# Optimization experiments

Measured on AMD Instinct MI355X. Metric: run time of the kernel, lower is better.

Reference implementation:

```python
import jax, jax.numpy as jnp
import numpy as np

EPS = 1e-8
WINDOW = 3      # config.router_window_size
TEMP = 1.0      # config.router_temp (> 0, so sqrt(D) fallback unused)
TOP_K = 2       # config.moe_top_k


def _routing_weights(x, prototypes):
    # L2-normalize router input per token (normalize_router_input=True)
    x = x / jnp.clip(jnp.linalg.norm(x, axis=-1, keepdims=True), EPS)
    # 'window' mode: causal moving average of size WINDOW along seq, with the
    # first token replicated WINDOW-1 times on the left (matches F.conv1d with
    # left pad of flat_input[:, :, [0]] and an averaging kernel).
    w = WINDOW
    padded = jnp.concatenate([jnp.repeat(x[:, :1], w - 1, axis=1), x], axis=1)  # [B, S+w-1, D]
    cs = jnp.concatenate(
        [jnp.zeros_like(padded[:, :1]), jnp.cumsum(padded, axis=1)], axis=1
    )  # [B, S+w, D]
    router_input = (cs[:, w:] - cs[:, :-w]) / w  # [B, S, D] moving mean
    # F.linear(router_input, prototypes): logits over experts
    logits = jnp.einsum('bsd,ed->bse', router_input, prototypes)  # [B, S, E]
    # softmax in float32 (F.softmax(..., dtype=torch.float))
    return jax.nn.softmax((logits / TEMP).astype(jnp.float32), axis=-1)


def setup_inputs() -> dict:
    key = jax.random.key(0)
    k1, k2 = jax.random.split(key)
    bs, sq, D, E = 8, 2048, 1024, 64
    x = jax.random.normal(k1, (bs, sq, D), dtype=jnp.float32)
    prototypes = jax.random.normal(k2, (E, D), dtype=jnp.float32) * 0.02
    attn_mask = jnp.ones((bs, sq), dtype=jnp.int32)
    return {"x": x, "prototypes": prototypes, "attn_mask": attn_mask}


def reference(x, prototypes, attn_mask):
    # attn_mask is all ones here; in 'window' mode it only feeds logging stats.
    routing_weights = _routing_weights(x, prototypes)          # [B, S, E]
    weights, modules = jax.lax.top_k(routing_weights, TOP_K)   # [B, S, K]
    weights = weights / weights.sum(axis=-1, keepdims=True)    # renormalize top-k
    return modules, weights
```

## Files before the change

kernel.cpp:

```cpp
#include <hip/hip_runtime.h>
#include <math.h>


#define BB 8
#define SS 2048
#define DD 1024
#define EE 64
#define EPSV 1e-8f

#define FMA4(A, s, P) \
  A.x += (s) * (P).x; A.y += (s) * (P).y; A.z += (s) * (P).z; A.w += (s) * (P).w;

__global__ __launch_bounds__(256) void repack_proto(
    const float* __restrict__ proto, float* __restrict__ ptt) {
  const int gid = blockIdx.x * 256 + threadIdx.x;
  const int d = gid >> 6;
  const int e = gid & 63;
  ptt[gid] = proto[(size_t)e * DD + d];
}

__global__ __launch_bounds__(256, 2) void router_dots(
    const float* __restrict__ x, const float* __restrict__ ptt,
    float* __restrict__ dots) {
  __shared__ float xt[4][16][36];
  __shared__ float B0[32][68];
  __shared__ float B1[32][68];
  __shared__ float nq[4][32];

  const int lane = threadIdx.x & 63;
  const int w    = __builtin_amdgcn_readfirstlane(threadIdx.x >> 6);
  const int b    = blockIdx.x >> 6;
  const int s0   = (blockIdx.x & 63) * 32;

  const int toks = lane & 31;
  const int kh   = lane >> 5;
  const int eg   = lane & 7;
  const int tg   = lane >> 3;

  const float* xb = x + ((size_t)b * SS + s0) * DD;
  const int kbase = w * 256;

  float4 acc0[4], acc1[4];
#pragma unroll
  for (int i = 0; i < 4; ++i) {
    acc0[i] = make_float4(0.f, 0.f, 0.f, 0.f);
    acc1[i] = make_float4(0.f, 0.f, 0.f, 0.f);
  }
  float q = 0.0f;

  for (int c = 0; c < 16; ++c) {
    const int dof = kbase + c * 16;
    const float* xs = xb + (size_t)toks * DD + dof + kh * 8;
    const float4 v0 = *(const float4*)(xs);
    const float4 v1 = *(const float4*)(xs + 4);
    q += v0.x * v0.x + v0.y * v0.y + v0.z * v0.z + v0.w * v0.w +
         v1.x * v1.x + v1.y * v1.y + v1.z * v1.z + v1.w * v1.w;
    xt[w][kh * 8 + 0][toks] = v0.x;
    xt[w][kh * 8 + 1][toks] = v0.y;
    xt[w][kh * 8 + 2][toks] = v0.z;
    xt[w][kh * 8 + 3][toks] = v0.w;
    xt[w][kh * 8 + 4][toks] = v1.x;
    xt[w][kh * 8 + 5][toks] = v1.y;
    xt[w][kh * 8 + 6][toks] = v1.z;
    xt[w][kh * 8 + 7][toks] = v1.w;
#pragma unroll
    for (int kk = 0; kk < 16; ++kk) {
      const float4 xf = *(const float4*)(&xt[w][kk][tg * 4]);
      const float* pr = ptt + (size_t)(dof + kk) * EE + eg * 8;
      const float4 p0 = *(const float4*)(pr);
      const float4 p1 = *(const float4*)(pr + 4);
      FMA4(acc0[0], xf.x, p0) FMA4(acc1[0], xf.x, p1)
      FMA4(acc0[1], xf.y, p0) FMA4(acc1[1], xf.y, p1)
      FMA4(acc0[2], xf.z, p0) FMA4(acc1[2], xf.z, p1)
      FMA4(acc0[3], xf.w, p0) FMA4(acc1[3], xf.w, p1)
    }
  }

  q += __shfl_xor(q, 32);
  if (kh == 0) nq[w][toks] = q;

#define WRB(B)                                                  \
  { _Pragma("unroll") for (int i = 0; i < 4; ++i) {             \
      *(float4*)(&(B)[tg * 4 + i][eg * 8])     = acc0[i];       \
      *(float4*)(&(B)[tg * 4 + i][eg * 8 + 4]) = acc1[i]; } }
#define ADDB(B)                                                 \
  { _Pragma("unroll") for (int i = 0; i < 4; ++i) {             \
      const float4 t0 = *(const float4*)(&(B)[tg * 4 + i][eg * 8]);     \
      const float4 t1 = *(const float4*)(&(B)[tg * 4 + i][eg * 8 + 4]); \
      acc0[i].x += t0.x; acc0[i].y += t0.y;                     \
      acc0[i].z += t0.z; acc0[i].w += t0.w;                     \
      acc1[i].x += t1.x; acc1[i].y += t1.y;                     \
      acc1[i].z += t1.z; acc1[i].w += t1.w; } }

  __syncthreads();
  if (w == 1) WRB(B0)
  if (w == 3) WRB(B1)
  __syncthreads();
  if (w == 0) ADDB(B0)
  if (w == 2) ADDB(B1)
  __syncthreads();
  if (w == 2) WRB(B0)
  __syncthreads();
  if (w == 0) {
    ADDB(B0)
#pragma unroll
    for (int i = 0; i < 4; ++i) {
      const int row = tg * 4 + i;
      const float qs = nq[0][row] + nq[1][row] + nq[2][row] + nq[3][row];
      const float inv = 1.0f / fmaxf(sqrtf(qs), EPSV);
      float4 o0, o1;
      o0.x = acc0[i].x * inv; o0.y = acc0[i].y * inv;
      o0.z = acc0[i].z * inv; o0.w = acc0[i].w * inv;
      o1.x = acc1[i].x * inv; o1.y = acc1[i].y * inv;
      o1.z = acc1[i].z * inv; o1.w = acc1[i].w * inv;
      float* dp = dots + ((size_t)b * SS + s0 + row) * EE + eg * 8;
      *(float4*)(dp)     = o0;
      *(float4*)(dp + 4) = o1;
    }
  }
}

#define T2UP(s, ei)                                            \
  if ((s) > v1) { v2 = v1; i2 = i1; v1 = (s); i1 = (ei); }     \
  else if ((s) > v2) { v2 = (s); i2 = (ei); }

__global__ __launch_bounds__(256) void router_top2(
    const float* __restrict__ dots, float* __restrict__ out) {
  const int gtid = blockIdx.x * 256 + threadIdx.x;
  const int tok  = gtid >> 1;
  const int h    = gtid & 1;
  const int b    = tok >> 11;
  const int sl   = tok & (SS - 1);
  const int r0   = (sl >= 2) ? sl - 2 : 0;
  const int r1   = (sl >= 1) ? sl - 1 : 0;

  const float* d0 = dots + ((size_t)b * SS + r0) * EE + h * 32;
  const float* d1 = dots + ((size_t)b * SS + r1) * EE + h * 32;
  const float* d2 = dots + ((size_t)b * SS + sl) * EE + h * 32;

  float v1 = -INFINITY, v2 = -INFINITY;
  int i1 = 0, i2 = 0;
#pragma unroll
  for (int qd = 0; qd < 8; ++qd) {
    const float4 a = *(const float4*)(d0 + qd * 4);
    const float4 c = *(const float4*)(d1 + qd * 4);
    const float4 e = *(const float4*)(d2 + qd * 4);
    const int e0 = h * 32 + qd * 4;
    float s;
    s = a.x + c.x + e.x; T2UP(s, e0 + 0)
    s = a.y + c.y + e.y; T2UP(s, e0 + 1)
    s = a.z + c.z + e.z; T2UP(s, e0 + 2)
    s = a.w + c.w + e.w; T2UP(s, e0 + 3)
  }

  {
    const float ov1 = __shfl_xor(v1, 1);
    const int   oi1 = __shfl_xor(i1, 1);
    const float ov2 = __shfl_xor(v2, 1);
    const int   oi2 = __shfl_xor(i2, 1);
    const bool o_beats = (ov1 > v1) || (ov1 == v1 && oi1 < i1);
    if (o_beats) {
      const bool v1_beats_o2 = (v1 > ov2) || (v1 == ov2 && i1 < oi2);
      v2 = v1_beats_o2 ? v1 : ov2;
      i2 = v1_beats_o2 ? i1 : oi2;
      v1 = ov1;
      i1 = oi1;
    } else {
      const bool o1_beats_v2 = (ov1 > v2) || (ov1 == v2 && oi1 < i2);
      if (o1_beats_v2) { v2 = ov1; i2 = oi1; }
    }
  }

  if (h == 0) {
    const float ex = expf((v2 - v1) * (1.0f / 3.0f));
    const float w1 = 1.0f / (1.0f + ex);
    const size_t o = (size_t)tok * 2;
    *(float2*)(out + o) = make_float2((float)i1, (float)i2);
    *(float2*)(out + (size_t)BB * SS * 2 + o) = make_float2(w1, ex * w1);
  }
}

extern "C" void kernel_launch(void* const* d_in, const int* in_sizes, int n_in,
                              void* d_out, int out_size, void* d_ws, size_t ws_size,
                              hipStream_t stream) {
  const float* x     = (const float*)d_in[0];
  const float* proto = (const float*)d_in[1];
  float* out  = (float*)d_out;
  float* ptt  = (float*)d_ws;
  float* dots = (float*)((char*)d_ws + (512 << 10));

  repack_proto<<<dim3(256), dim3(256), 0, stream>>>(proto, ptt);
  router_dots<<<dim3(512), dim3(256), 0, stream>>>(x, ptt, dots);
  router_top2<<<dim3(128), dim3(256), 0, stream>>>(dots, out);
}
```

Before: 136.1 us.

## Split K across 8 waves with double-buffered x tiles and prototype prefetch

The dot kernel now runs 512 threads per block, splitting the 1024-wide reduction over 8 waves of 128 columns each instead of 4 waves of 256. Each wave double-buffers its transposed x tile in shared memory, loading the next chunk while computing the current one. It also keeps a 4-deep register ring of prototype rows prefetched ahead of use. The goal is to hide global load latency and raise the number of waves in flight, at the cost of a deeper cross-wave reduction tree with more barriers and more register and LDS pressure.

```diff
diff --git a/kernel.cpp b/kernel.cpp
--- a/kernel.cpp
+++ b/kernel.cpp
@@ -8,8 +8,14 @@
 #define EE 64
 #define EPSV 1e-8f
 
+#define NW 8
+#define KSL 128
+#define NCHK 8
+
 #define FMA4(A, s, P) \
   A.x += (s) * (P).x; A.y += (s) * (P).y; A.z += (s) * (P).z; A.w += (s) * (P).w;
+
+#define SUMSQ4(v) ((v).x * (v).x + (v).y * (v).y + (v).z * (v).z + (v).w * (v).w)
 
 __global__ __launch_bounds__(256) void repack_proto(
     const float* __restrict__ proto, float* __restrict__ ptt) {
@@ -19,13 +25,12 @@
   ptt[gid] = proto[(size_t)e * DD + d];
 }
 
-__global__ __launch_bounds__(256, 2) void router_dots(
+__global__ __launch_bounds__(512, 4) void router_dots(
     const float* __restrict__ x, const float* __restrict__ ptt,
     float* __restrict__ dots) {
-  __shared__ float xt[4][16][36];
-  __shared__ float B0[32][68];
-  __shared__ float B1[32][68];
-  __shared__ float nq[4][32];
+  __shared__ float xt[NW][2][16][36];
+  __shared__ float B[4][32][68];
+  __shared__ float nq[NW][32];
 
   const int lane = threadIdx.x & 63;
   const int w    = __builtin_amdgcn_readfirstlane(threadIdx.x >> 6);
@@ -38,7 +43,7 @@
   const int tg   = lane >> 3;
 
   const float* xb = x + ((size_t)b * SS + s0) * DD;
-  const int kbase = w * 256;
+  const int kbase = w * KSL;
 
   float4 acc0[4], acc1[4];
 #pragma unroll
@@ -48,65 +53,105 @@
   }
   float q = 0.0f;
 
-  for (int c = 0; c < 16; ++c) {
-    const int dof = kbase + c * 16;
-    const float* xs = xb + (size_t)toks * DD + dof + kh * 8;
-    const float4 v0 = *(const float4*)(xs);
-    const float4 v1 = *(const float4*)(xs + 4);
-    q += v0.x * v0.x + v0.y * v0.y + v0.z * v0.z + v0.w * v0.w +
-         v1.x * v1.x + v1.y * v1.y + v1.z * v1.z + v1.w * v1.w;
-    xt[w][kh * 8 + 0][toks] = v0.x;
-    xt[w][kh * 8 + 1][toks] = v0.y;
-    xt[w][kh * 8 + 2][toks] = v0.z;
-    xt[w][kh * 8 + 3][toks] = v0.w;
-    xt[w][kh * 8 + 4][toks] = v1.x;
-    xt[w][kh * 8 + 5][toks] = v1.y;
-    xt[w][kh * 8 + 6][toks] = v1.z;
-    xt[w][kh * 8 + 7][toks] = v1.w;
+  {
+    const float* xs = xb + (size_t)toks * DD + kbase + kh * 8;
+    const float4 va = *(const float4*)(xs);
+    const float4 vb = *(const float4*)(xs + 4);
+    q += SUMSQ4(va) + SUMSQ4(vb);
+    float* dstc = &xt[w][0][0][toks];
+    dstc[(kh * 8 + 0) * 36] = va.x;
+    dstc[(kh * 8 + 1) * 36] = va.y;
+    dstc[(kh * 8 + 2) * 36] = va.z;
+    dstc[(kh * 8 + 3) * 36] = va.w;
+    dstc[(kh * 8 + 4) * 36] = vb.x;
+    dstc[(kh * 8 + 5) * 36] = vb.y;
+    dstc[(kh * 8 + 6) * 36] = vb.z;
+    dstc[(kh * 8 + 7) * 36] = vb.w;
+  }
+
+  float4 pp0[4], pp1[4];
+#pragma unroll
+  for (int r = 0; r < 4; ++r) {
+    const float* pr = ptt + (size_t)(kbase + r) * EE + eg * 8;
+    pp0[r] = *(const float4*)(pr);
+    pp1[r] = *(const float4*)(pr + 4);
+  }
+
+  for (int c = 0; c < NCHK; ++c) {
+    const int cur = c & 1;
+    float4 na, nb;
+    if (c + 1 < NCHK) {
+      const float* xs = xb + (size_t)toks * DD + kbase + (c + 1) * 16 + kh * 8;
+      na = *(const float4*)(xs);
+      nb = *(const float4*)(xs + 4);
+    }
 #pragma unroll
     for (int kk = 0; kk < 16; ++kk) {
-      const float4 xf = *(const float4*)(&xt[w][kk][tg * 4]);
-      const float* pr = ptt + (size_t)(dof + kk) * EE + eg * 8;
-      const float4 p0 = *(const float4*)(pr);
-      const float4 p1 = *(const float4*)(pr + 4);
+      const int slot = kk & 3;
+      const float4 xf = *(const float4*)(&xt[w][cur][kk][tg * 4]);
+      const float4 p0 = pp0[slot];
+      const float4 p1 = pp1[slot];
+      int kpre = kbase + c * 16 + kk + 4;
+      if (kpre > kbase + KSL - 1) kpre = kbase + KSL - 1;
+      const float* pr = ptt + (size_t)kpre * EE + eg * 8;
+      pp0[slot] = *(const float4*)(pr);
+      pp1[slot] = *(const float4*)(pr + 4);
       FMA4(acc0[0], xf.x, p0) FMA4(acc1[0], xf.x, p1)
       FMA4(acc0[1], xf.y, p0) FMA4(acc1[1], xf.y, p1)
       FMA4(acc0[2], xf.z, p0) FMA4(acc1[2], xf.z, p1)
       FMA4(acc0[3], xf.w, p0) FMA4(acc1[3], xf.w, p1)
     }
+    if (c + 1 < NCHK) {
+      q += SUMSQ4(na) + SUMSQ4(nb);
+      float* dstc = &xt[w][cur ^ 1][0][toks];
+      dstc[(kh * 8 + 0) * 36] = na.x;
+      dstc[(kh * 8 + 1) * 36] = na.y;
+      dstc[(kh * 8 + 2) * 36] = na.z;
+      dstc[(kh * 8 + 3) * 36] = na.w;
+      dstc[(kh * 8 + 4) * 36] = nb.x;
+      dstc[(kh * 8 + 5) * 36] = nb.y;
+      dstc[(kh * 8 + 6) * 36] = nb.z;
+      dstc[(kh * 8 + 7) * 36] = nb.w;
+    }
   }
 
   q += __shfl_xor(q, 32);
   if (kh == 0) nq[w][toks] = q;
 
-#define WRB(B)                                                  \
+#define WRB(R)                                                  \
   { _Pragma("unroll") for (int i = 0; i < 4; ++i) {             \
-      *(float4*)(&(B)[tg * 4 + i][eg * 8])     = acc0[i];       \
-      *(float4*)(&(B)[tg * 4 + i][eg * 8 + 4]) = acc1[i]; } }
-#define ADDB(B)                                                 \
+      *(float4*)(&(R)[tg * 4 + i][eg * 8])     = acc0[i];       \
+      *(float4*)(&(R)[tg * 4 + i][eg * 8 + 4]) = acc1[i]; } }
+#define ADDB(R)                                                 \
   { _Pragma("unroll") for (int i = 0; i < 4; ++i) {             \
-      const float4 t0 = *(const float4*)(&(B)[tg * 4 + i][eg * 8]);     \
-      const float4 t1 = *(const float4*)(&(B)[tg * 4 + i][eg * 8 + 4]); \
+      const float4 t0 = *(const float4*)(&(R)[tg * 4 + i][eg * 8]);     \
+      const float4 t1 = *(const float4*)(&(R)[tg * 4 + i][eg * 8 + 4]); \
       acc0[i].x += t0.x; acc0[i].y += t0.y;                     \
       acc0[i].z += t0.z; acc0[i].w += t0.w;                     \
       acc1[i].x += t1.x; acc1[i].y += t1.y;                     \
       acc1[i].z += t1.z; acc1[i].w += t1.w; } }
 
   __syncthreads();
-  if (w == 1) WRB(B0)
-  if (w == 3) WRB(B1)
-  __syncthreads();
-  if (w == 0) ADDB(B0)
-  if (w == 2) ADDB(B1)
-  __syncthreads();
-  if (w == 2) WRB(B0)
+  if (w & 1) WRB(B[w >> 1])
+  __syncthreads();
+  if (!(w & 1)) ADDB(B[w >> 1])
+  __syncthreads();
+  if (w == 2) WRB(B[0])
+  if (w == 6) WRB(B[1])
+  __syncthreads();
+  if (w == 0) ADDB(B[0])
+  if (w == 4) ADDB(B[1])
+  __syncthreads();
+  if (w == 4) WRB(B[0])
   __syncthreads();
   if (w == 0) {
-    ADDB(B0)
+    ADDB(B[0])
 #pragma unroll
     for (int i = 0; i < 4; ++i) {
       const int row = tg * 4 + i;
-      const float qs = nq[0][row] + nq[1][row] + nq[2][row] + nq[3][row];
+      float qs = 0.0f;
+#pragma unroll
+      for (int wv = 0; wv < NW; ++wv) qs += nq[wv][row];
       const float inv = 1.0f / fmaxf(sqrtf(qs), EPSV);
       float4 o0, o1;
       o0.x = acc0[i].x * inv; o0.y = acc0[i].y * inv;
@@ -190,6 +235,6 @@
   float* dots = (float*)((char*)d_ws + (512 << 10));
 
   repack_proto<<<dim3(256), dim3(256), 0, stream>>>(proto, ptt);
-  router_dots<<<dim3(512), dim3(256), 0, stream>>>(x, ptt, dots);
+  router_dots<<<dim3(512), dim3(512), 0, stream>>>(x, ptt, dots);
   router_top2<<<dim3(128), dim3(256), 0, stream>>>(dots, out);
 }
```

New measurement: 187.7 us. +37.9%, slower.
